# Kernel optimization log

Measured on AMD Instinct MI355X. Metric: run time of the kernel, lower is better.

The kernel has to match this reference:

```python
import jax, jax.numpy as jnp
import numpy as np

B, C, H, W = 8, 32, 256, 448


def setup_inputs() -> dict:
    key = jax.random.key(0)
    k1, k2 = jax.random.split(key)
    input1 = jax.random.normal(k1, (B, C, H, W), dtype=jnp.float32)
    input2 = jax.random.normal(k2, (B, 2, H, W), dtype=jnp.float32)  # flow (u, v)
    return {"input1": input1, "input2": input2, "kernel_size": 1}


def _forward_splat(input1, input2):
    """Forward warp: splat each source pixel to (x+u, y+v) with bilinear weights,
    accumulating via scatter-add (kernel_size=1 -> 2x2 bilinear footprint)."""
    b, c, h, w = input1.shape
    u = input2[:, 0]  # [B,H,W] horizontal flow
    v = input2[:, 1]  # [B,H,W] vertical flow
    xs = jnp.arange(w, dtype=input2.dtype)
    ys = jnp.arange(h, dtype=input2.dtype)
    tx = xs[None, None, :] + u  # target x, [B,H,W]
    ty = ys[None, :, None] + v  # target y, [B,H,W]
    x0 = jnp.floor(tx).astype(jnp.int32)
    y0 = jnp.floor(ty).astype(jnp.int32)
    fx = tx - x0.astype(tx.dtype)
    fy = ty - y0.astype(ty.dtype)

    vals = input1.transpose(0, 2, 3, 1).reshape(b * h * w, c)  # [BHW, C]
    out = jnp.zeros((b * h * w, c), dtype=input1.dtype)
    batch_off = (jnp.arange(b, dtype=jnp.int32) * (h * w))[:, None, None]

    for dx, dy in ((0, 0), (1, 0), (0, 1), (1, 1)):
        xx = x0 + dx
        yy = y0 + dy
        wx = fx if dx == 1 else (1.0 - fx)
        wy = fy if dy == 1 else (1.0 - fy)
        wgt = wx * wy  # [B,H,W]
        valid = (xx >= 0) & (xx < w) & (yy >= 0) & (yy < h)
        wgt = jnp.where(valid, wgt, 0.0)
        idx = batch_off + jnp.clip(yy, 0, h - 1) * w + jnp.clip(xx, 0, w - 1)
        out = out.at[idx.reshape(-1)].add(wgt.reshape(-1, 1) * vals)

    return out.reshape(b, h, w, c).transpose(0, 3, 1, 2)


def reference(input1, input2, kernel_size):
    # kernel_size=1 corresponds to the standard bilinear (2x2) splat footprint.
    return _forward_splat(input1, input2)
```

## Files before the change

### kernel.cpp

```cpp
#include <hip/hip_runtime.h>
#include <hip/hip_fp16.h>

constexpr int B = 8;
constexpr int C = 32;
constexpr int H = 256;
constexpr int W = 448;
constexpr int HW = H * W;

constexpr int TW  = 32;
constexpr int TH  = 8;
constexpr int RAD = 3;
constexpr int WX  = TW + 2 * RAD;
constexpr int WY  = TH + 2 * RAD;
constexpr int NSRC = WX * WY;
constexpr int NT  = 256;
constexpr int SITER = (NSRC + NT - 1) / NT;

static __device__ __forceinline__ unsigned pkrtz(float a, float b) {
    return __builtin_bit_cast(unsigned, __builtin_amdgcn_cvt_pkrtz(a, b));
}

static __device__ __forceinline__ __half2 h2(unsigned u) {
    union { unsigned u; __half2 h; } x;
    x.u = u;
    return x.h;
}

__global__ __launch_bounds__(NT)
void splat_out(const float* __restrict__ in1,
               const float* __restrict__ flow,
               float* __restrict__ out,
               unsigned* __restrict__ wcnt,
               unsigned* __restrict__ wlist,
               unsigned cap) {
    __shared__ unsigned char geomR8[NSRC];
    __shared__ uint2         geomW[NSRC];
    __shared__ uint4         valV[4 * NSRC];

    int bid = blockIdx.x;
    int b = bid & 7;
    int t = bid >> 3;
    int ty = t / 14;
    int tx = t - ty * 14;
    int ox = tx * TW, oy = ty * TH;
    int tid = threadIdx.x;
    int qlx = tid & 31, qly = tid >> 5;
    int qx = ox + qlx, qy = oy + qly;

    int sg[SITER];
    const int fbase = b * 2 * HW;
#pragma unroll
    for (int j = 0; j < SITER; ++j) {
        int i = tid + j * NT;
        if (i < NSRC) {
            int wy = i / WX, wx = i - wy * WX;
            int sx = ox + wx - RAD, sy = oy + wy - RAD;
            int cx = min(max(sx, 0), W - 1), cy = min(max(sy, 0), H - 1);
            int g = cy * W + cx;
            sg[j] = g;
            unsigned gr = 0xFFu;
            uint2 wd = make_uint2(0u, 0u);
            if (sx == cx && sy == cy) {
                float u = flow[fbase + g];
                float v = flow[fbase + g + HW];
                float txf = (float)sx + u;
                float tyf = (float)sy + v;
                float x0f = floorf(txf), y0f = floorf(tyf);
                int rx = (int)x0f - sx, ry = (int)y0f - sy;
                if (rx >= -RAD && rx <= RAD - 1 && ry >= -RAD && ry <= RAD - 1) {
                    float fx = txf - x0f, fy = tyf - y0f;
                    wd.x = pkrtz((1.f - fx) * (1.f - fy), fx * (1.f - fy));
                    wd.y = pkrtz((1.f - fx) * fy,         fx * fy);
                    gr = (unsigned)(rx + RAD) | ((unsigned)(ry + RAD) << 3);
                } else if (wx >= RAD && wx < RAD + TW && wy >= RAD && wy < RAD + TH) {
                    unsigned slot = atomicAdd(wcnt, 1u);
                    if (slot < cap) wlist[slot] = ((unsigned)b << 17) | (unsigned)g;
                }
            }
            geomR8[i] = (unsigned char)gr;
            geomW[i]  = wd;
        } else {
            sg[j] = -1;
        }
    }
    __syncthreads();

    const float* inb = in1 + (size_t)b * C * HW;
#pragma unroll
    for (int j = 0; j < SITER; ++j) {
        int i = tid + j * NT;
        if (i < NSRC) {
            const float* p = inb + sg[j];
#pragma unroll
            for (int q = 0; q < 4; ++q) {
                const float* pq = p + (size_t)(8 * q) * HW;
                uint4 vq;
                vq.x = pkrtz(pq[0],              pq[(size_t)HW]);
                vq.y = pkrtz(pq[(size_t)2 * HW], pq[(size_t)3 * HW]);
                vq.z = pkrtz(pq[(size_t)4 * HW], pq[(size_t)5 * HW]);
                vq.w = pkrtz(pq[(size_t)6 * HW], pq[(size_t)7 * HW]);
                valV[q * NSRC + i] = vq;
            }
        }
    }

    unsigned long long mAll = 0ull, mDx = 0ull, mDy = 0ull;
    const int qbase = (qly + RAD) * WX + (qlx + RAD);
#pragma unroll
    for (int dy = -RAD; dy <= RAD; ++dy) {
#pragma unroll
        for (int dx = -RAD; dx <= RAD; ++dx) {
            unsigned g = geomR8[qbase + dy * WX + dx];
            int tX = (int)(g & 7u) + dx;
            int tY = (int)((g >> 3) & 0x1Fu) + dy;
            bool mx = (unsigned)(tX - 2) <= 1u;
            bool my = (unsigned)(tY - 2) <= 1u;
            const int j = (dy + RAD) * 8 + (dx + RAD);
            unsigned long long bit = (mx && my) ? (1ull << j) : 0ull;
            mAll |= bit;
            if (!(tX & 1)) mDx |= bit;
            if (!(tY & 1)) mDy |= bit;
        }
    }
    __syncthreads();

    __half2 acc2[16];
#pragma unroll
    for (int k = 0; k < 16; ++k) acc2[k] = h2(0u);

    const int joff = 3 * WX + 3;
    unsigned long long m = mAll;
    while (m) {
        int j = (int)__builtin_ctzll(m);
        m &= m - 1;
        int wi = qbase + ((j >> 3) * WX + (j & 7)) - joff;
        unsigned dyy = (unsigned)(mDy >> j) & 1u;
        unsigned dxx = (unsigned)(mDx >> j) & 1u;
        uint2 wd2 = geomW[wi];
        unsigned wd = dyy ? wd2.y : wd2.x;
        unsigned hw = (wd >> (16u * dxx)) & 0xFFFFu;
        __half2 w2 = h2(hw | (hw << 16));
        uint4 v0 = valV[0 * NSRC + wi];
        uint4 v1 = valV[1 * NSRC + wi];
        uint4 v2 = valV[2 * NSRC + wi];
        uint4 v3 = valV[3 * NSRC + wi];
        acc2[0]  = __hfma2(h2(v0.x), w2, acc2[0]);
        acc2[1]  = __hfma2(h2(v0.y), w2, acc2[1]);
        acc2[2]  = __hfma2(h2(v0.z), w2, acc2[2]);
        acc2[3]  = __hfma2(h2(v0.w), w2, acc2[3]);
        acc2[4]  = __hfma2(h2(v1.x), w2, acc2[4]);
        acc2[5]  = __hfma2(h2(v1.y), w2, acc2[5]);
        acc2[6]  = __hfma2(h2(v1.z), w2, acc2[6]);
        acc2[7]  = __hfma2(h2(v1.w), w2, acc2[7]);
        acc2[8]  = __hfma2(h2(v2.x), w2, acc2[8]);
        acc2[9]  = __hfma2(h2(v2.y), w2, acc2[9]);
        acc2[10] = __hfma2(h2(v2.z), w2, acc2[10]);
        acc2[11] = __hfma2(h2(v2.w), w2, acc2[11]);
        acc2[12] = __hfma2(h2(v3.x), w2, acc2[12]);
        acc2[13] = __hfma2(h2(v3.y), w2, acc2[13]);
        acc2[14] = __hfma2(h2(v3.z), w2, acc2[14]);
        acc2[15] = __hfma2(h2(v3.w), w2, acc2[15]);
    }

    float* o = out + (size_t)b * C * HW + qy * W + qx;
#pragma unroll
    for (int k = 0; k < 16; ++k) {
        int c0 = 8 * (k >> 2) + 2 * (k & 3);
        float2 f = __half22float2(acc2[k]);
        o[(size_t)c0 * HW]       = f.x;
        o[(size_t)(c0 + 1) * HW] = f.y;
    }
}

__global__ void outlier_list(const float* __restrict__ in1,
                             const float* __restrict__ flow,
                             float* __restrict__ out,
                             const unsigned* __restrict__ wcnt,
                             const unsigned* __restrict__ wlist,
                             unsigned cap) {
    unsigned n = *wcnt;
    if (n > cap) return;
    unsigned total = n * 8u;
    for (unsigned idx = blockIdx.x * blockDim.x + threadIdx.x;
         idx < total; idx += gridDim.x * blockDim.x) {
        unsigned e = wlist[idx >> 3];
        int c0 = (int)(idx & 7u) * 4;
        int bb = (int)(e >> 17);
        int p  = (int)(e & 0x1FFFFu);
        int y = p / W, x = p - y * W;

        float u = flow[(bb * 2 + 0) * HW + p];
        float v = flow[(bb * 2 + 1) * HW + p];
        float txf = (float)x + u;
        float tyf = (float)y + v;
        float fx0 = floorf(txf), fy0 = floorf(tyf);
        int x0 = (int)fx0, y0 = (int)fy0;
        float fx = txf - fx0, fy = tyf - fy0;
        float w00 = (1.0f - fx) * (1.0f - fy);
        float w10 = fx * (1.0f - fy);
        float w01 = (1.0f - fx) * fy;
        float w11 = fx * fy;
        bool vx0 = (x0 >= 0) && (x0 < W);
        bool vx1 = (x0 + 1 >= 0) && (x0 + 1 < W);
        bool vy0 = (y0 >= 0) && (y0 < H);
        bool vy1 = (y0 + 1 >= 0) && (y0 + 1 < H);
        long o00 = (long)y0 * W + x0;

        const float* src  = in1 + (size_t)bb * C * HW + (size_t)c0 * HW + p;
        float*       dstb = out + (size_t)bb * C * HW + (size_t)c0 * HW;
        for (int c = 0; c < 4; ++c) {
            float val = src[(size_t)c * HW];
            float* ob = dstb + (size_t)c * HW;
            if (vx0 && vy0) atomicAdd(ob + o00,         w00 * val);
            if (vx1 && vy0) atomicAdd(ob + o00 + 1,     w10 * val);
            if (vx0 && vy1) atomicAdd(ob + o00 + W,     w01 * val);
            if (vx1 && vy1) atomicAdd(ob + o00 + W + 1, w11 * val);
        }
    }
}

__global__ void outlier_fallback(const float* __restrict__ in1,
                                 const float* __restrict__ flow,
                                 float* __restrict__ out,
                                 const unsigned* __restrict__ wcnt,
                                 unsigned cap) {
    if (*wcnt <= cap) return;
    int npix = B * HW;
    for (int idx = blockIdx.x * blockDim.x + threadIdx.x;
         idx < npix; idx += gridDim.x * blockDim.x) {
        int b = idx / HW;
        int p = idx - b * HW;
        int y = p / W, x = p - y * W;
        float u = flow[(b * 2 + 0) * HW + p];
        float v = flow[(b * 2 + 1) * HW + p];
        float txf = (float)x + u;
        float tyf = (float)y + v;
        float fx0 = floorf(txf), fy0 = floorf(tyf);
        int x0 = (int)fx0, y0 = (int)fy0;
        int rx = x0 - x, ry = y0 - y;
        bool handled = (rx >= -RAD) && (rx <= RAD - 1) &&
                       (ry >= -RAD) && (ry <= RAD - 1);
        if (handled) continue;
        float fx = txf - fx0, fy = tyf - fy0;
        float w00 = (1.0f - fx) * (1.0f - fy);
        float w10 = fx * (1.0f - fy);
        float w01 = (1.0f - fx) * fy;
        float w11 = fx * fy;
        bool vx0 = (x0 >= 0) && (x0 < W);
        bool vx1 = (x0 + 1 >= 0) && (x0 + 1 < W);
        bool vy0 = (y0 >= 0) && (y0 < H);
        bool vy1 = (y0 + 1 >= 0) && (y0 + 1 < H);
        long o00 = (long)y0 * W + x0;
        const float* src = in1 + (size_t)b * C * HW + p;
        float* dstb = out + (size_t)b * C * HW;
        for (int c = 0; c < C; ++c) {
            float val = src[(size_t)c * HW];
            float* ob = dstb + (size_t)c * HW;
            if (vx0 && vy0) atomicAdd(ob + o00,         w00 * val);
            if (vx1 && vy0) atomicAdd(ob + o00 + 1,     w10 * val);
            if (vx0 && vy1) atomicAdd(ob + o00 + W,     w01 * val);
            if (vx1 && vy1) atomicAdd(ob + o00 + W + 1, w11 * val);
        }
    }
}

extern "C" void kernel_launch(void* const* d_in, const int* in_sizes, int n_in,
                              void* d_out, int out_size, void* d_ws, size_t ws_size,
                              hipStream_t stream) {
    const float* in1  = (const float*)d_in[0];
    const float* flow = (const float*)d_in[1];
    float* out = (float*)d_out;

    unsigned* wcnt  = (unsigned*)d_ws;
    unsigned* wlist = wcnt + 4;
    unsigned cap = 0;
    if (ws_size >= 64) {
        size_t c = ws_size / sizeof(unsigned) - 4;
        cap = (c > 0x7FFFFFFFull) ? 0x7FFFFFFFu : (unsigned)c;
    }

    hipMemsetAsync(wcnt, 0, sizeof(unsigned), stream);

    int nblocks = B * (H / TH) * (W / TW);
    splat_out<<<nblocks, NT, 0, stream>>>(in1, flow, out, wcnt, wlist, cap);

    outlier_list<<<256, 256, 0, stream>>>(in1, flow, out, wcnt, wlist, cap);
    outlier_fallback<<<256, 256, 0, stream>>>(in1, flow, out, wcnt, cap);
}
```

Measured before the change: 115.5 us.

## Halve shared value buffer with two channel passes and build masks via atomicOr

New measurement: 113.3 us. No clear change (-1.9%).

```diff
diff --git a/kernel.cpp b/kernel.cpp
--- a/kernel.cpp
+++ b/kernel.cpp
@@ -33,9 +33,11 @@
                unsigned* __restrict__ wcnt,
                unsigned* __restrict__ wlist,
                unsigned cap) {
-    __shared__ unsigned char geomR8[NSRC];
-    __shared__ uint2         geomW[NSRC];
-    __shared__ uint4         valV[4 * NSRC];
+    __shared__ unsigned long long cellMask[TW * TH];
+    __shared__ unsigned char     geomR8[NSRC];
+    __shared__ uint2             geomW[NSRC];
+    __shared__ uint4             valA[NSRC];
+    __shared__ uint4             valB[NSRC];
 
     int bid = blockIdx.x;
     int b = bid & 7;
@@ -46,6 +48,9 @@
     int tid = threadIdx.x;
     int qlx = tid & 31, qly = tid >> 5;
     int qx = ox + qlx, qy = oy + qly;
+
+    cellMask[tid] = 0ull;
+    __syncthreads();
 
     int sg[SITER];
     const int fbase = b * 2 * HW;
@@ -72,6 +77,19 @@
                     wd.x = pkrtz((1.f - fx) * (1.f - fy), fx * (1.f - fy));
                     wd.y = pkrtz((1.f - fx) * fy,         fx * fy);
                     gr = (unsigned)(rx + RAD) | ((unsigned)(ry + RAD) << 3);
+                    int lx0 = wx + rx;
+                    int ly0 = wy + ry;
+#pragma unroll
+                    for (int corner = 0; corner < 4; ++corner) {
+                        int dxx = corner & 1, dyy = corner >> 1;
+                        int ccx = lx0 + dxx - RAD;
+                        int ccy = ly0 + dyy - RAD;
+                        if ((unsigned)ccx < (unsigned)TW &&
+                            (unsigned)ccy < (unsigned)TH) {
+                            int jb = (3 - (ry + dyy)) * 8 + (3 - (rx + dxx));
+                            atomicOr(&cellMask[ccy * TW + ccx], 1ull << jb);
+                        }
+                    }
                 } else if (wx >= RAD && wx < RAD + TW && wy >= RAD && wy < RAD + TH) {
                     unsigned slot = atomicAdd(wcnt, 1u);
                     if (slot < cap) wlist[slot] = ((unsigned)b << 17) | (unsigned)g;
@@ -83,7 +101,6 @@
             sg[j] = -1;
         }
     }
-    __syncthreads();
 
     const float* inb = in1 + (size_t)b * C * HW;
 #pragma unroll
@@ -91,84 +108,115 @@
         int i = tid + j * NT;
         if (i < NSRC) {
             const float* p = inb + sg[j];
-#pragma unroll
-            for (int q = 0; q < 4; ++q) {
-                const float* pq = p + (size_t)(8 * q) * HW;
-                uint4 vq;
-                vq.x = pkrtz(pq[0],              pq[(size_t)HW]);
-                vq.y = pkrtz(pq[(size_t)2 * HW], pq[(size_t)3 * HW]);
-                vq.z = pkrtz(pq[(size_t)4 * HW], pq[(size_t)5 * HW]);
-                vq.w = pkrtz(pq[(size_t)6 * HW], pq[(size_t)7 * HW]);
-                valV[q * NSRC + i] = vq;
-            }
-        }
-    }
-
-    unsigned long long mAll = 0ull, mDx = 0ull, mDy = 0ull;
+            valA[i] = make_uint4(pkrtz(p[0],               p[(size_t)HW]),
+                                 pkrtz(p[(size_t)2 * HW],  p[(size_t)3 * HW]),
+                                 pkrtz(p[(size_t)4 * HW],  p[(size_t)5 * HW]),
+                                 pkrtz(p[(size_t)6 * HW],  p[(size_t)7 * HW]));
+            const float* p8 = p + (size_t)8 * HW;
+            valB[i] = make_uint4(pkrtz(p8[0],              p8[(size_t)HW]),
+                                 pkrtz(p8[(size_t)2 * HW], p8[(size_t)3 * HW]),
+                                 pkrtz(p8[(size_t)4 * HW], p8[(size_t)5 * HW]),
+                                 pkrtz(p8[(size_t)6 * HW], p8[(size_t)7 * HW]));
+        }
+    }
+    __syncthreads();
+
+    const unsigned long long m0 = cellMask[qly * TW + qlx];
     const int qbase = (qly + RAD) * WX + (qlx + RAD);
-#pragma unroll
-    for (int dy = -RAD; dy <= RAD; ++dy) {
-#pragma unroll
-        for (int dx = -RAD; dx <= RAD; ++dx) {
-            unsigned g = geomR8[qbase + dy * WX + dx];
-            int tX = (int)(g & 7u) + dx;
-            int tY = (int)((g >> 3) & 0x1Fu) + dy;
-            bool mx = (unsigned)(tX - 2) <= 1u;
-            bool my = (unsigned)(tY - 2) <= 1u;
-            const int j = (dy + RAD) * 8 + (dx + RAD);
-            unsigned long long bit = (mx && my) ? (1ull << j) : 0ull;
-            mAll |= bit;
-            if (!(tX & 1)) mDx |= bit;
-            if (!(tY & 1)) mDy |= bit;
+    float* outp = out + (size_t)b * C * HW + qy * W + qx;
+
+    {
+        __half2 acc2[8];
+#pragma unroll
+        for (int k = 0; k < 8; ++k) acc2[k] = h2(0u);
+        unsigned long long m = m0;
+        while (m) {
+            int j = (int)__builtin_ctzll(m);
+            m &= m - 1;
+            int dx = (j & 7) - 3, dy = (j >> 3) - 3;
+            int wi = qbase + dy * WX + dx;
+            unsigned g8 = geomR8[wi];
+            int tX = (int)(g8 & 7u) + dx;
+            int tY = (int)(g8 >> 3) + dy;
+            unsigned dxx = (tX == 2), dyy = (tY == 2);
+            uint2 wd2 = geomW[wi];
+            unsigned wd = dyy ? wd2.y : wd2.x;
+            unsigned hw = (wd >> (16u * dxx)) & 0xFFFFu;
+            __half2 w2 = h2(hw | (hw << 16));
+            uint4 a = valA[wi];
+            uint4 bb = valB[wi];
+            acc2[0] = __hfma2(h2(a.x),  w2, acc2[0]);
+            acc2[1] = __hfma2(h2(a.y),  w2, acc2[1]);
+            acc2[2] = __hfma2(h2(a.z),  w2, acc2[2]);
+            acc2[3] = __hfma2(h2(a.w),  w2, acc2[3]);
+            acc2[4] = __hfma2(h2(bb.x), w2, acc2[4]);
+            acc2[5] = __hfma2(h2(bb.y), w2, acc2[5]);
+            acc2[6] = __hfma2(h2(bb.z), w2, acc2[6]);
+            acc2[7] = __hfma2(h2(bb.w), w2, acc2[7]);
+        }
+#pragma unroll
+        for (int k = 0; k < 8; ++k) {
+            float2 f = __half22float2(acc2[k]);
+            outp[(size_t)(2 * k) * HW]     = f.x;
+            outp[(size_t)(2 * k + 1) * HW] = f.y;
         }
     }
     __syncthreads();
 
-    __half2 acc2[16];
-#pragma unroll
-    for (int k = 0; k < 16; ++k) acc2[k] = h2(0u);
-
-    const int joff = 3 * WX + 3;
-    unsigned long long m = mAll;
-    while (m) {
-        int j = (int)__builtin_ctzll(m);
-        m &= m - 1;
-        int wi = qbase + ((j >> 3) * WX + (j & 7)) - joff;
-        unsigned dyy = (unsigned)(mDy >> j) & 1u;
-        unsigned dxx = (unsigned)(mDx >> j) & 1u;
-        uint2 wd2 = geomW[wi];
-        unsigned wd = dyy ? wd2.y : wd2.x;
-        unsigned hw = (wd >> (16u * dxx)) & 0xFFFFu;
-        __half2 w2 = h2(hw | (hw << 16));
-        uint4 v0 = valV[0 * NSRC + wi];
-        uint4 v1 = valV[1 * NSRC + wi];
-        uint4 v2 = valV[2 * NSRC + wi];
-        uint4 v3 = valV[3 * NSRC + wi];
-        acc2[0]  = __hfma2(h2(v0.x), w2, acc2[0]);
-        acc2[1]  = __hfma2(h2(v0.y), w2, acc2[1]);
-        acc2[2]  = __hfma2(h2(v0.z), w2, acc2[2]);
-        acc2[3]  = __hfma2(h2(v0.w), w2, acc2[3]);
-        acc2[4]  = __hfma2(h2(v1.x), w2, acc2[4]);
-        acc2[5]  = __hfma2(h2(v1.y), w2, acc2[5]);
-        acc2[6]  = __hfma2(h2(v1.z), w2, acc2[6]);
-        acc2[7]  = __hfma2(h2(v1.w), w2, acc2[7]);
-        acc2[8]  = __hfma2(h2(v2.x), w2, acc2[8]);
-        acc2[9]  = __hfma2(h2(v2.y), w2, acc2[9]);
-        acc2[10] = __hfma2(h2(v2.z), w2, acc2[10]);
-        acc2[11] = __hfma2(h2(v2.w), w2, acc2[11]);
-        acc2[12] = __hfma2(h2(v3.x), w2, acc2[12]);
-        acc2[13] = __hfma2(h2(v3.y), w2, acc2[13]);
-        acc2[14] = __hfma2(h2(v3.z), w2, acc2[14]);
-        acc2[15] = __hfma2(h2(v3.w), w2, acc2[15]);
-    }
-
-    float* o = out + (size_t)b * C * HW + qy * W + qx;
-#pragma unroll
-    for (int k = 0; k < 16; ++k) {
-        int c0 = 8 * (k >> 2) + 2 * (k & 3);
-        float2 f = __half22float2(acc2[k]);
-        o[(size_t)c0 * HW]       = f.x;
-        o[(size_t)(c0 + 1) * HW] = f.y;
+#pragma unroll
+    for (int j = 0; j < SITER; ++j) {
+        int i = tid + j * NT;
+        if (i < NSRC) {
+            const float* p = inb + sg[j] + (size_t)16 * HW;
+            valA[i] = make_uint4(pkrtz(p[0],               p[(size_t)HW]),
+                                 pkrtz(p[(size_t)2 * HW],  p[(size_t)3 * HW]),
+                                 pkrtz(p[(size_t)4 * HW],  p[(size_t)5 * HW]),
+                                 pkrtz(p[(size_t)6 * HW],  p[(size_t)7 * HW]));
+            const float* p8 = p + (size_t)8 * HW;
+            valB[i] = make_uint4(pkrtz(p8[0],              p8[(size_t)HW]),
+                                 pkrtz(p8[(size_t)2 * HW], p8[(size_t)3 * HW]),
+                                 pkrtz(p8[(size_t)4 * HW], p8[(size_t)5 * HW]),
+                                 pkrtz(p8[(size_t)6 * HW], p8[(size_t)7 * HW]));
+        }
+    }
+    __syncthreads();
+
+    {
+        __half2 acc2[8];
+#pragma unroll
+        for (int k = 0; k < 8; ++k) acc2[k] = h2(0u);
+        unsigned long long m = m0;
+        while (m) {
+            int j = (int)__builtin_ctzll(m);
+            m &= m - 1;
+            int dx = (j & 7) - 3, dy = (j >> 3) - 3;
+            int wi = qbase + dy * WX + dx;
+            unsigned g8 = geomR8[wi];
+            int tX = (int)(g8 & 7u) + dx;
+            int tY = (int)(g8 >> 3) + dy;
+            unsigned dxx = (tX == 2), dyy = (tY == 2);
+            uint2 wd2 = geomW[wi];
+            unsigned wd = dyy ? wd2.y : wd2.x;
+            unsigned hw = (wd >> (16u * dxx)) & 0xFFFFu;
+            __half2 w2 = h2(hw | (hw << 16));
+            uint4 a = valA[wi];
+            uint4 bb = valB[wi];
+            acc2[0] = __hfma2(h2(a.x),  w2, acc2[0]);
+            acc2[1] = __hfma2(h2(a.y),  w2, acc2[1]);
+            acc2[2] = __hfma2(h2(a.z),  w2, acc2[2]);
+            acc2[3] = __hfma2(h2(a.w),  w2, acc2[3]);
+            acc2[4] = __hfma2(h2(bb.x), w2, acc2[4]);
+            acc2[5] = __hfma2(h2(bb.y), w2, acc2[5]);
+            acc2[6] = __hfma2(h2(bb.z), w2, acc2[6]);
+            acc2[7] = __hfma2(h2(bb.w), w2, acc2[7]);
+        }
+        float* o1 = outp + (size_t)16 * HW;
+#pragma unroll
+        for (int k = 0; k < 8; ++k) {
+            float2 f = __half22float2(acc2[k]);
+            o1[(size_t)(2 * k) * HW]     = f.x;
+            o1[(size_t)(2 * k + 1) * HW] = f.y;
+        }
     }
 }
 
```
